# Kernel optimization log

Measured on AMD Instinct MI355X. Metric: run time of the kernel, lower is better.

The kernel has to match this reference:

```python
import jax, jax.numpy as jnp
import numpy as np
from math import pi

RADIUS = 40.0  # radius_scale
B, N = 1, 512


def map_polar_sqr(x, y, eps=1e-9):
    r = jnp.sqrt(x * x + y * y + eps)
    cond1 = (x == 0.0) & (y == 0.0)
    cond2 = (jnp.abs(y) <= jnp.abs(x)) & (~cond1)
    sx = jnp.where(x == 0.0, 1.0, x)  # safe denominators
    sy = jnp.where(y == 0.0, 1.0, y)
    c = 4.0 / pi
    x2 = jnp.sign(x) * r
    y2 = c * jnp.sign(x) * r * jnp.arctan(y / sx)
    x3 = c * jnp.sign(y) * r * jnp.arctan(x / sy)
    y3 = jnp.sign(y) * r
    x_out = jnp.where(cond1, 0.0, jnp.where(cond2, x2, x3))
    y_out = jnp.where(cond1, 0.0, jnp.where(cond2, y2, y3))
    return x_out, y_out


def axis_weights(g, size):
    # F.grid_sample bilinear, align_corners=False, padding_mode='zeros':
    # pixel coord = ((g+1)*size - 1)/2; linear weights on floor/floor+1,
    # out-of-range taps drop to zero automatically (idx only covers 0..size-1).
    c = ((g + 1.0) * size - 1.0) * 0.5
    i0 = jnp.floor(c)
    f = c - i0
    idx = jnp.arange(size, dtype=g.dtype)
    m0 = (idx == i0[..., None]).astype(g.dtype)
    m1 = (idx == i0[..., None] + 1.0).astype(g.dtype)
    return (1.0 - f)[..., None] * m0 + f[..., None] * m1  # [..., size]


def cts_conv(kernel, field, center, feat, mask, radius):
    # kernel: [o, i, kD, kH, kW]; field/center: [b, n/m, 3]; feat: [b, n, i]; mask: [b, n, 1]
    rel = (field[:, None] - center[:, :, None]) / radius            # [b,m,n,3]
    r2 = jnp.sum(rel * rel, -1)                                     # [b,m,n]
    att = jax.nn.relu((1.0 - r2) ** 3)[..., None] * mask[:, None]   # [b,m,n,1]
    xs, ys = map_polar_sqr(rel[..., 0], rel[..., 1])
    zs = rel[..., 2]
    kD, kH, kW = kernel.shape[2:]
    # grid_sample coord order: grid x -> W (last dim), y -> H, z -> D (first spatial dim)
    wz = axis_weights(zs, kD)
    wy = axis_weights(ys, kH)
    wx = axis_weights(xs, kW)
    w = jnp.einsum('bmnz,bmny,bmnx->bmnzyx', wz, wy, wx)
    w = w.reshape(*w.shape[:3], -1)                                 # [b,m,n,g=kD*kH*kW]
    fa = feat[:, None] * att                                        # [b,m,n,i]
    # exact trilinear interp + neighbor contraction without the [b,m,n,o,i] tensor:
    t = jnp.einsum('bmng,bmni->bmgi', w, fa)                        # [b,m,g,i]
    K = kernel.reshape(kernel.shape[0], kernel.shape[1], -1)        # [o,i,g]
    return jnp.einsum('bmgi,oig->bmo', t, K)


def setup_inputs() -> dict:
    key = jax.random.key(0)
    ks = jax.random.split(key, 24)

    def kern(k, o, i):
        return (jax.random.uniform(k, (o, i, 4, 4, 4), dtype=jnp.float32) - 0.5) / float(np.sqrt(i))

    def lin(kw, kb, o, i):
        return (jax.random.normal(kw, (o, i), dtype=jnp.float32) * 0.05,
                jax.random.normal(kb, (o,), dtype=jnp.float32) * 0.05)

    p = jax.random.normal(ks[0], (B, N, 3), dtype=jnp.float32) * 20.0
    v = jax.random.normal(ks[1], (B, N, 3), dtype=jnp.float32)
    other_feats = jax.random.normal(ks[2], (B, N, 62), dtype=jnp.float32)
    fluid_mask = jnp.ones((B, N, 1), dtype=jnp.float32)

    k_fluid = kern(ks[3], 32, 66)
    Wf, bf = lin(ks[4], ks[5], 32, 66)
    k1 = kern(ks[6], 64, 64); W1, b1 = lin(ks[7], ks[8], 64, 64)
    k2 = kern(ks[9], 64, 64); W2, b2 = lin(ks[10], ks[11], 64, 64)
    k3 = kern(ks[12], 64, 64); W3, b3 = lin(ks[13], ks[14], 64, 64)
    k4 = kern(ks[15], 6, 64); W4, b4 = lin(ks[16], ks[17], 6, 64)
    return dict(p=p, v=v, other_feats=other_feats, fluid_mask=fluid_mask,
                k_fluid=k_fluid, Wf=Wf, bf=bf,
                k1=k1, W1=W1, b1=b1, k2=k2, W2=W2, b2=b2,
                k3=k3, W3=W3, b3=b3, k4=k4, W4=W4, b4=b4)


def reference(p, v, other_feats, fluid_mask, k_fluid, Wf, bf,
              k1, W1, b1, k2, W2, b2, k3, W3, b3, k4, W4, b4):
    feats0 = jnp.concatenate([jnp.ones_like(p[..., :1]), v, other_feats], -1)  # [b,n,66]
    oc = cts_conv(k_fluid, p, p, feats0, fluid_mask, RADIUS)
    od = feats0 @ Wf.T + bf
    output = jnp.concatenate([oc, od], -1)  # [b,n,64]
    for k, W, bb in ((k1, W1, b1), (k2, W2, b2), (k3, W3, b3), (k4, W4, b4)):
        h = jax.nn.relu(output)
        oc = cts_conv(k, p, p, h, fluid_mask, RADIUS)
        od = h @ W.T + bb
        if od.shape[-1] == output.shape[-1]:
            output = oc + od + output
        else:
            output = oc + od
    return output  # [b,n,6]
```

## Files before the change

kernel.cpp:

```cpp
#include <hip/hip_runtime.h>

typedef _Float16 f16;
typedef _Float16 f16x8 __attribute__((ext_vector_type(8)));
typedef float f32x4 __attribute__((ext_vector_type(4)));

#define INV_R (1.0f / 40.0f)

#define OFF_HT   0u
#define OFF_B0   81920u
#define OFF_K0   82176u
#define OFF_K1   635136u
#define OFF_K2   1167616u
#define OFF_K3   1700096u
#define OFF_K4   2232576u
#define OFF_TA   2365696u
#define OFF_TB   6789376u
#define OFF_OA   11049216u
#define OFF_OB   11180288u
#define OFF_BAR  11311360u

#define PREP_TOTAL 1231936
#define NBLK 512

__device__ __forceinline__ unsigned bar_ld(unsigned* p) {
  return __hip_atomic_load(p, __ATOMIC_RELAXED, __HIP_MEMORY_SCOPE_AGENT);
}
__device__ void gridbar(unsigned* bar, int phase) {
  __syncthreads();
  if (threadIdx.x == 0) {
    int bid = blockIdx.x;
    int xcd = bid & 7;
    unsigned* xcnt = bar + xcd * 32 + phase;
    unsigned* xrel = bar + 256 + xcd * 32 + phase;
    unsigned* gcnt = bar + 512 + phase;
    unsigned* grel = bar + 544 + phase;
    __threadfence();
    __hip_atomic_fetch_add(xcnt, 1u, __ATOMIC_RELAXED, __HIP_MEMORY_SCOPE_AGENT);
    if (bid < 8) {
      while (bar_ld(xcnt) < (NBLK / 8)) __builtin_amdgcn_s_sleep(2);
      __hip_atomic_fetch_add(gcnt, 1u, __ATOMIC_RELAXED, __HIP_MEMORY_SCOPE_AGENT);
      if (bid == 0) {
        while (bar_ld(gcnt) < 8u) __builtin_amdgcn_s_sleep(2);
        __hip_atomic_store(grel, 1u, __ATOMIC_RELAXED, __HIP_MEMORY_SCOPE_AGENT);
      } else {
        while (bar_ld(grel) == 0u) __builtin_amdgcn_s_sleep(2);
      }
      __hip_atomic_store(xrel, 1u, __ATOMIC_RELAXED, __HIP_MEMORY_SCOPE_AGENT);
    } else {
      while (bar_ld(xrel) == 0u) __builtin_amdgcn_s_sleep(4);
    }
    __threadfence();
  }
  __syncthreads();
}

__device__ __forceinline__ float feats0_val(int ch, int n, const float* v, const float* other) {
  if (ch == 0) return 1.0f;
  if (ch < 4) return v[n * 3 + (ch - 1)];
  return other[n * 62 + (ch - 4)];
}

__device__ void prep_body(const float* __restrict__ v, const float* __restrict__ other,
                          const float* __restrict__ kf, const float* __restrict__ Wf,
                          const float* __restrict__ bf,
                          const float* __restrict__ k1, const float* __restrict__ W1,
                          const float* __restrict__ k2, const float* __restrict__ W2,
                          const float* __restrict__ k3, const float* __restrict__ W3,
                          const float* __restrict__ k4, const float* __restrict__ W4,
                          char* __restrict__ ws) {
  for (int idx0 = blockIdx.x * 256 + threadIdx.x; idx0 < PREP_TOTAL; idx0 += 512 * 256) {
    int idx = idx0;
    if (idx < 40960) {
      int i = idx >> 9, n = idx & 511;
      float val = (i < 66) ? feats0_val(i, n, v, other) : 0.0f;
      ((f16*)(ws + OFF_HT))[idx] = (f16)val;
      continue;
    }
    idx -= 40960;
    if (idx < 49152) {
      int m = idx / 96, j = idx % 96;
      float val = (j < 66) ? feats0_val(j, m, v, other) : 0.0f;
      ((f16*)(ws + OFF_TA))[m * 4320 + 4224 + j] = (f16)val;
      continue;
    }
    idx -= 49152;
    if (idx < 276480) {
      int o = idx / 4320, k = idx % 4320;
      float val = 0.0f;
      if (o < 32) { if (k < 4224) val = kf[o * 4224 + k]; }
      else if (k >= 4224 && k < 4290) val = Wf[(o - 32) * 66 + (k - 4224)];
      ((f16*)(ws + OFF_K0))[idx] = (f16)val;
      continue;
    }
    idx -= 276480;
    if (idx < 798720) {
      int which = idx / 266240, e = idx % 266240;
      const float* kk = which == 0 ? k1 : (which == 1 ? k2 : k3);
      const float* WW = which == 0 ? W1 : (which == 1 ? W2 : W3);
      int o = e / 4160, k = e % 4160;
      float val = (k < 4096) ? kk[o * 4096 + k] : WW[o * 64 + (k - 4096)];
      ((f16*)(ws + OFF_K1 + (unsigned)which * 532480u))[e] = (f16)val;
      continue;
    }
    idx -= 798720;
    if (idx < 66560) {
      int o = idx / 4160, k = idx % 4160;
      float val = 0.0f;
      if (o < 6) val = (k < 4096) ? k4[o * 4096 + k] : W4[o * 64 + (k - 4096)];
      ((f16*)(ws + OFF_K4))[idx] = (f16)val;
      continue;
    }
    idx -= 66560;
    if (idx < 64) ((float*)(ws + OFF_B0))[idx] = (idx < 32) ? 0.0f : bf[idx - 32];
  }
}

__device__ __forceinline__ float atan_poly(float t) {
  float t2 = t * t;
  float p = -0.0117212f;
  p = p * t2 + 0.05265332f;
  p = p * t2 - 0.11643287f;
  p = p * t2 + 0.19354346f;
  p = p * t2 - 0.33262347f;
  p = p * t2 + 0.99997726f;
  return t * p;
}

__device__ __forceinline__ void axis_w(float g, int& i0c, int& i1c, float& w0, float& w1) {
  float c = 2.0f * g + 1.5f;
  float fl = floorf(c);
  float f = c - fl;
  int i0 = (int)fl;
  w0 = (i0 >= 0 && i0 <= 3) ? (1.0f - f) : 0.0f;
  w1 = (i0 >= -1 && i0 <= 2) ? f : 0.0f;
  i0c = min(max(i0, 0), 3);
  i1c = min(max(i0 + 1, 0), 3);
}

template<int CI, int ITILES, int KDIM>
__device__ void stage1_body(const float* __restrict__ p, const float* __restrict__ mask,
                            const f16* __restrict__ hT, f16* __restrict__ tout,
                            f16* __restrict__ Wlds) {
  int tid = threadIdx.x;
  int m = blockIdx.x;
  int4* wz4 = (int4*)Wlds;
  int4 zero4 = make_int4(0, 0, 0, 0);
  #pragma unroll
  for (int i = 0; i < 16; ++i) wz4[tid + i * 256] = zero4;
  float pmx = p[m * 3 + 0], pmy = p[m * 3 + 1], pmz = p[m * 3 + 2];
  __syncthreads();
  #pragma unroll
  for (int rep = 0; rep < 2; ++rep) {
    int n = rep * 256 + tid;
    float x = (p[n * 3 + 0] - pmx) * INV_R;
    float y = (p[n * 3 + 1] - pmy) * INV_R;
    float z = (p[n * 3 + 2] - pmz) * INV_R;
    float r2 = x * x + y * y + z * z;
    float q = 1.0f - r2;
    float att = (q > 0.0f) ? q * q * q * mask[n] : 0.0f;
    bool c1 = (x == 0.0f) && (y == 0.0f);
    bool c2 = (fabsf(y) <= fabsf(x)) && !c1;
    float r = sqrtf(x * x + y * y + 1e-9f);
    float num = c2 ? y : x;
    float den = c2 ? x : y;
    float a = atan_poly(num / den);
    float s2 = copysignf(r, x), s3 = copysignf(r, y);
    const float C4PI = 1.2732395447351628f;
    float xs = c1 ? 0.0f : (c2 ? s2 : C4PI * s3 * a);
    float ys = c1 ? 0.0f : (c2 ? C4PI * s2 * a : s3);
    float zs = z;
    int iz0, iz1, iy0, iy1, ix0, ix1;
    float wz0, wz1, wy0, wy1, wx0, wx1;
    axis_w(zs, iz0, iz1, wz0, wz1);
    axis_w(ys, iy0, iy1, wy0, wy1);
    axis_w(xs, ix0, ix1, wx0, wx1);
    wz0 *= att; wz1 *= att;
    int gz[2] = {iz0 * 16, iz1 * 16};
    int gy[2] = {iy0 * 4, iy1 * 4};
    int gx[2] = {ix0, ix1};
    float wzv[2] = {wz0, wz1}, wyv[2] = {wy0, wy1}, wxv[2] = {wx0, wx1};
    #pragma unroll
    for (int za = 0; za < 2; ++za)
      #pragma unroll
      for (int ya = 0; ya < 2; ++ya)
        #pragma unroll
        for (int xa = 0; xa < 2; ++xa) {
          float w = wzv[za] * wyv[ya] * wxv[xa];
          if (w != 0.0f) {
            int g = gz[za] + gy[ya] + gx[xa];
            Wlds[g * 512 + (n ^ ((g & 7) << 3))] = (f16)w;
          }
        }
  }
  __syncthreads();
  int wave = tid >> 6, lane = tid & 63;
  int row = lane & 15, kgrp = lane >> 4;
  int grow = wave * 16 + row;
  f32x4 acc[ITILES];
  #pragma unroll
  for (int it = 0; it < ITILES; ++it) acc[it] = f32x4{0.f, 0.f, 0.f, 0.f};
  for (int k0 = 0; k0 < 512; k0 += 32) {
    int n0 = k0 + kgrp * 8;
    f16x8 afrag = *(f16x8*)&Wlds[grow * 512 + (n0 ^ ((grow & 7) << 3))];
    #pragma unroll
    for (int it = 0; it < ITILES; ++it) {
      int icol = it * 16 + row;
      f16x8 bfrag = *(const f16x8*)&hT[icol * 512 + n0];
      acc[it] = __builtin_amdgcn_mfma_f32_16x16x32_f16(afrag, bfrag, acc[it], 0, 0, 0);
    }
  }
  int g4 = wave * 16 + kgrp * 4;
  #pragma unroll
  for (int it = 0; it < ITILES; ++it) {
    int icol = it * 16 + row;
    if (icol < CI) {
      union { f16 h[4]; ushort4 u; } cv;
      #pragma unroll
      for (int r = 0; r < 4; ++r) cv.h[r] = (f16)acc[it][r];
      *(ushort4*)&tout[(size_t)m * KDIM + icol * 64 + g4] = cv.u;
    }
  }
}

template<int KDIM, bool RES, bool FINAL>
__device__ void stage2_body(const f16* __restrict__ t, const f16* __restrict__ Kf,
                            const float* __restrict__ bias, const float* __restrict__ res,
                            float* __restrict__ out32, f16* __restrict__ hT,
                            f16* __restrict__ tnext, float* __restrict__ dout,
                            float* __restrict__ red) {
  int b = blockIdx.x;
  if (b >= 128) return;
  int mtile = b >> 2, otile = b & 3;
  constexpr int KSTEPS = KDIM / 32;
  int tid = threadIdx.x;
  int kpart = tid >> 6, lane = tid & 63;
  int row = lane & 15, kgrp = lane >> 4;
  int mrow = mtile * 16 + row;
  int ocol = otile * 16 + row;
  f32x4 acc = {0.f, 0.f, 0.f, 0.f};
  for (int ks = kpart; ks < KSTEPS; ks += 4) {
    int k0 = ks * 32 + kgrp * 8;
    f16x8 afrag = *(const f16x8*)&t[(size_t)mrow * KDIM + k0];
    f16x8 bfrag = *(const f16x8*)&Kf[(size_t)ocol * KDIM + k0];
    acc = __builtin_amdgcn_mfma_f32_16x16x32_f16(afrag, bfrag, acc, 0, 0, 0);
  }
  if (kpart > 0) {
    #pragma unroll
    for (int r = 0; r < 4; ++r)
      red[(kpart - 1) * 256 + (kgrp * 4 + r) * 16 + row] = acc[r];
  }
  __syncthreads();
  if (kpart == 0) {
    #pragma unroll
    for (int kw = 0; kw < 3; ++kw)
      #pragma unroll
      for (int r = 0; r < 4; ++r)
        acc[r] += red[kw * 256 + (kgrp * 4 + r) * 16 + row];
    #pragma unroll
    for (int r = 0; r < 4; ++r) {
      int mm = mtile * 16 + kgrp * 4 + r;
      int oo = otile * 16 + row;
      if (FINAL) {
        if (oo < 6) dout[mm * 6 + oo] = acc[r] + bias[oo];
      } else {
        float val = acc[r] + bias[oo];
        if (RES) val += res[mm * 64 + oo];
        out32[mm * 64 + oo] = val;
        float h = fmaxf(val, 0.0f);
        hT[oo * 512 + mm] = (f16)h;
        tnext[(size_t)mm * 4160 + 4096 + oo] = (f16)h;
      }
    }
  }
}

__global__ __launch_bounds__(256, 2) void mega_kernel(
    const float* p, const float* v, const float* other, const float* mask,
    const float* kf, const float* Wf, const float* bf,
    const float* k1, const float* W1, const float* b1,
    const float* k2, const float* W2, const float* b2,
    const float* k3, const float* W3, const float* b3,
    const float* k4, const float* W4, const float* b4,
    float* dout, char* ws) {
  __shared__ int4 smem4[4096];
  f16* Wlds = (f16*)smem4;
  float* red = (float*)smem4;
  unsigned* bar = (unsigned*)(ws + OFF_BAR);

  f16* hT        = (f16*)(ws + OFF_HT);
  float* bias0   = (float*)(ws + OFF_B0);
  const f16* K0p = (const f16*)(ws + OFF_K0);
  const f16* K1p = (const f16*)(ws + OFF_K1);
  const f16* K2p = (const f16*)(ws + OFF_K2);
  const f16* K3p = (const f16*)(ws + OFF_K3);
  const f16* K4p = (const f16*)(ws + OFF_K4);
  f16* tA   = (f16*)(ws + OFF_TA);
  f16* tB   = (f16*)(ws + OFF_TB);
  float* outA = (float*)(ws + OFF_OA);
  float* outB = (float*)(ws + OFF_OB);

  prep_body(v, other, kf, Wf, bf, k1, W1, k2, W2, k3, W3, k4, W4, ws);
  gridbar(bar, 0);
  stage1_body<66, 5, 4320>(p, mask, hT, tA, Wlds);
  gridbar(bar, 1);
  stage2_body<4320, false, false>(tA, K0p, bias0, nullptr, outA, hT, tB, nullptr, red);
  gridbar(bar, 2);
  stage1_body<64, 4, 4160>(p, mask, hT, tB, Wlds);
  gridbar(bar, 3);
  stage2_body<4160, true, false>(tB, K1p, b1, outA, outB, hT, tA, nullptr, red);
  gridbar(bar, 4);
  stage1_body<64, 4, 4160>(p, mask, hT, tA, Wlds);
  gridbar(bar, 5);
  stage2_body<4160, true, false>(tA, K2p, b2, outB, outA, hT, tB, nullptr, red);
  gridbar(bar, 6);
  stage1_body<64, 4, 4160>(p, mask, hT, tB, Wlds);
  gridbar(bar, 7);
  stage2_body<4160, true, false>(tB, K3p, b3, outA, outB, hT, tA, nullptr, red);
  gridbar(bar, 8);
  stage1_body<64, 4, 4160>(p, mask, hT, tA, Wlds);
  gridbar(bar, 9);
  stage2_body<4160, false, true>(tA, K4p, b4, nullptr, nullptr, nullptr, nullptr, dout, red);
}

__global__ void prep_kernel_g(const float* v, const float* other,
                              const float* kf, const float* Wf, const float* bf,
                              const float* k1, const float* W1,
                              const float* k2, const float* W2,
                              const float* k3, const float* W3,
                              const float* k4, const float* W4, char* ws) {
  prep_body(v, other, kf, Wf, bf, k1, W1, k2, W2, k3, W3, k4, W4, ws);
}

template<int CI, int ITILES, int KDIM>
__global__ __launch_bounds__(256) void stage1_kernel_g(const float* p, const float* mask,
                                                       const f16* hT, f16* tout) {
  __shared__ int4 smem4[4096];
  stage1_body<CI, ITILES, KDIM>(p, mask, hT, tout, (f16*)smem4);
}

template<int KDIM, bool RES, bool FINAL>
__global__ __launch_bounds__(256) void stage2_kernel_g(const f16* t, const f16* Kf,
                                                       const float* bias, const float* res,
                                                       float* out32, f16* hT, f16* tnext,
                                                       float* dout) {
  __shared__ float red[3 * 256];
  stage2_body<KDIM, RES, FINAL>(t, Kf, bias, res, out32, hT, tnext, dout, red);
}

extern "C" void kernel_launch(void* const* d_in, const int* in_sizes, int n_in,
                              void* d_out, int out_size, void* d_ws, size_t ws_size,
                              hipStream_t stream) {
  const float* p     = (const float*)d_in[0];
  const float* v     = (const float*)d_in[1];
  const float* other = (const float*)d_in[2];
  const float* mask  = (const float*)d_in[3];
  const float* kf    = (const float*)d_in[4];
  const float* Wf    = (const float*)d_in[5];
  const float* bf    = (const float*)d_in[6];
  const float* k1    = (const float*)d_in[7];
  const float* W1    = (const float*)d_in[8];
  const float* b1    = (const float*)d_in[9];
  const float* k2    = (const float*)d_in[10];
  const float* W2    = (const float*)d_in[11];
  const float* b2    = (const float*)d_in[12];
  const float* k3    = (const float*)d_in[13];
  const float* W3    = (const float*)d_in[14];
  const float* b3    = (const float*)d_in[15];
  const float* k4    = (const float*)d_in[16];
  const float* W4    = (const float*)d_in[17];
  const float* b4    = (const float*)d_in[18];
  float* dout = (float*)d_out;
  char* ws = (char*)d_ws;
  (void)in_sizes; (void)n_in; (void)out_size; (void)ws_size;

  f16* hT        = (f16*)(ws + OFF_HT);
  float* bias0   = (float*)(ws + OFF_B0);
  const f16* K0p = (const f16*)(ws + OFF_K0);
  const f16* K1p = (const f16*)(ws + OFF_K1);
  const f16* K2p = (const f16*)(ws + OFF_K2);
  const f16* K3p = (const f16*)(ws + OFF_K3);
  const f16* K4p = (const f16*)(ws + OFF_K4);
  f16* tA   = (f16*)(ws + OFF_TA);
  f16* tB   = (f16*)(ws + OFF_TB);
  float* outA = (float*)(ws + OFF_OA);
  float* outB = (float*)(ws + OFF_OB);

  int maxb = 0;
  hipError_t e1 = hipOccupancyMaxActiveBlocksPerMultiprocessor(
      &maxb, (const void*)mega_kernel, 256, 0);
  if (e1 == hipSuccess && maxb >= 2) {
    hipMemsetAsync(ws + OFF_BAR, 0, 2304, stream);
    void* args[] = {
      (void*)&p, (void*)&v, (void*)&other, (void*)&mask,
      (void*)&kf, (void*)&Wf, (void*)&bf,
      (void*)&k1, (void*)&W1, (void*)&b1,
      (void*)&k2, (void*)&W2, (void*)&b2,
      (void*)&k3, (void*)&W3, (void*)&b3,
      (void*)&k4, (void*)&W4, (void*)&b4,
      (void*)&dout, (void*)&ws
    };
    hipError_t e2 = hipLaunchCooperativeKernel((const void*)mega_kernel, dim3(NBLK),
                                               dim3(256), args, 0, stream);
    if (e2 == hipSuccess) return;
  }

  prep_kernel_g<<<512, 256, 0, stream>>>(v, other, kf, Wf, bf, k1, W1, k2, W2,
                                         k3, W3, k4, W4, ws);
  stage1_kernel_g<66, 5, 4320><<<512, 256, 0, stream>>>(p, mask, hT, tA);
  stage2_kernel_g<4320, false, false><<<128, 256, 0, stream>>>(tA, K0p, bias0, nullptr,
                                                               outA, hT, tB, nullptr);
  stage1_kernel_g<64, 4, 4160><<<512, 256, 0, stream>>>(p, mask, hT, tB);
  stage2_kernel_g<4160, true, false><<<128, 256, 0, stream>>>(tB, K1p, b1, outA,
                                                              outB, hT, tA, nullptr);
  stage1_kernel_g<64, 4, 4160><<<512, 256, 0, stream>>>(p, mask, hT, tA);
  stage2_kernel_g<4160, true, false><<<128, 256, 0, stream>>>(tA, K2p, b2, outB,
                                                              outA, hT, tB, nullptr);
  stage1_kernel_g<64, 4, 4160><<<512, 256, 0, stream>>>(p, mask, hT, tB);
  stage2_kernel_g<4160, true, false><<<128, 256, 0, stream>>>(tB, K3p, b3, outA,
                                                              outB, hT, tA, nullptr);
  stage1_kernel_g<64, 4, 4160><<<512, 256, 0, stream>>>(p, mask, hT, tA);
  stage2_kernel_g<4160, false, true><<<128, 256, 0, stream>>>(tA, K4p, b4, nullptr,
                                                              nullptr, nullptr, nullptr, dout);
}
```

Baseline: 187.3 us.

## Fuse per-layer gather and kernel contraction into one stage with LDS-resident intermediates

```diff
diff --git a/kernel.cpp b/kernel.cpp
--- a/kernel.cpp
+++ b/kernel.cpp
@@ -1,26 +1,25 @@
 #include <hip/hip_runtime.h>
 
 typedef _Float16 f16;
+typedef _Float16 f16x2 __attribute__((ext_vector_type(2)));
 typedef _Float16 f16x8 __attribute__((ext_vector_type(8)));
 typedef float f32x4 __attribute__((ext_vector_type(4)));
 
 #define INV_R (1.0f / 40.0f)
-
-#define OFF_HT   0u
-#define OFF_B0   81920u
-#define OFF_K0   82176u
-#define OFF_K1   635136u
-#define OFF_K2   1167616u
-#define OFF_K3   1700096u
-#define OFF_K4   2232576u
-#define OFF_TA   2365696u
-#define OFF_TB   6789376u
-#define OFF_OA   11049216u
-#define OFF_OB   11180288u
-#define OFF_BAR  11311360u
-
-#define PREP_TOTAL 1231936
-#define NBLK 512
+#define NBLK 256
+
+#define OFF_HTA  0u
+#define OFF_HTB  81920u
+#define OFF_KT0  163840u
+#define OFF_KT1  720896u
+#define OFF_KT2  1253376u
+#define OFF_KT3  1785856u
+#define OFF_KT4  2318336u
+#define OFF_HG   2850816u
+#define OFF_OG   2916352u
+#define OFF_BAR  3047424u
+
+#define PREP_TOTAL 1384448
 
 __device__ __forceinline__ unsigned bar_ld(unsigned* p) {
   return __hip_atomic_load(p, __ATOMIC_RELAXED, __HIP_MEMORY_SCOPE_AGENT);
@@ -59,62 +58,6 @@
   if (ch < 4) return v[n * 3 + (ch - 1)];
   return other[n * 62 + (ch - 4)];
 }
-
-__device__ void prep_body(const float* __restrict__ v, const float* __restrict__ other,
-                          const float* __restrict__ kf, const float* __restrict__ Wf,
-                          const float* __restrict__ bf,
-                          const float* __restrict__ k1, const float* __restrict__ W1,
-                          const float* __restrict__ k2, const float* __restrict__ W2,
-                          const float* __restrict__ k3, const float* __restrict__ W3,
-                          const float* __restrict__ k4, const float* __restrict__ W4,
-                          char* __restrict__ ws) {
-  for (int idx0 = blockIdx.x * 256 + threadIdx.x; idx0 < PREP_TOTAL; idx0 += 512 * 256) {
-    int idx = idx0;
-    if (idx < 40960) {
-      int i = idx >> 9, n = idx & 511;
-      float val = (i < 66) ? feats0_val(i, n, v, other) : 0.0f;
-      ((f16*)(ws + OFF_HT))[idx] = (f16)val;
-      continue;
-    }
-    idx -= 40960;
-    if (idx < 49152) {
-      int m = idx / 96, j = idx % 96;
-      float val = (j < 66) ? feats0_val(j, m, v, other) : 0.0f;
-      ((f16*)(ws + OFF_TA))[m * 4320 + 4224 + j] = (f16)val;
-      continue;
-    }
-    idx -= 49152;
-    if (idx < 276480) {
-      int o = idx / 4320, k = idx % 4320;
-      float val = 0.0f;
-      if (o < 32) { if (k < 4224) val = kf[o * 4224 + k]; }
-      else if (k >= 4224 && k < 4290) val = Wf[(o - 32) * 66 + (k - 4224)];
-      ((f16*)(ws + OFF_K0))[idx] = (f16)val;
-      continue;
-    }
-    idx -= 276480;
-    if (idx < 798720) {
-      int which = idx / 266240, e = idx % 266240;
-      const float* kk = which == 0 ? k1 : (which == 1 ? k2 : k3);
-      const float* WW = which == 0 ? W1 : (which == 1 ? W2 : W3);
-      int o = e / 4160, k = e % 4160;
-      float val = (k < 4096) ? kk[o * 4096 + k] : WW[o * 64 + (k - 4096)];
-      ((f16*)(ws + OFF_K1 + (unsigned)which * 532480u))[e] = (f16)val;
-      continue;
-    }
-    idx -= 798720;
-    if (idx < 66560) {
-      int o = idx / 4160, k = idx % 4160;
-      float val = 0.0f;
-      if (o < 6) val = (k < 4096) ? k4[o * 4096 + k] : W4[o * 64 + (k - 4096)];
-      ((f16*)(ws + OFF_K4))[idx] = (f16)val;
-      continue;
-    }
-    idx -= 66560;
-    if (idx < 64) ((float*)(ws + OFF_B0))[idx] = (idx < 32) ? 0.0f : bf[idx - 32];
-  }
-}
-
 __device__ __forceinline__ float atan_poly(float t) {
   float t2 = t * t;
   float p = -0.0117212f;
@@ -125,7 +68,6 @@
   p = p * t2 + 0.99997726f;
   return t * p;
 }
-
 __device__ __forceinline__ void axis_w(float g, int& i0c, int& i1c, float& w0, float& w1) {
   float c = 2.0f * g + 1.5f;
   float fl = floorf(c);
@@ -136,145 +78,213 @@
   i0c = min(max(i0, 0), 3);
   i1c = min(max(i0 + 1, 0), 3);
 }
-
-template<int CI, int ITILES, int KDIM>
-__device__ void stage1_body(const float* __restrict__ p, const float* __restrict__ mask,
-                            const f16* __restrict__ hT, f16* __restrict__ tout,
-                            f16* __restrict__ Wlds) {
-  int tid = threadIdx.x;
-  int m = blockIdx.x;
-  int4* wz4 = (int4*)Wlds;
-  int4 zero4 = make_int4(0, 0, 0, 0);
+__device__ __forceinline__ float dot2f(f16x2 a, f16x2 b, float c) {
+#if defined(__has_builtin) && __has_builtin(__builtin_amdgcn_fdot2)
+  return __builtin_amdgcn_fdot2(a, b, c, false);
+#else
+  return c + (float)a[0] * (float)b[0] + (float)a[1] * (float)b[1];
+#endif
+}
+
+__device__ void prep_body(const float* __restrict__ v, const float* __restrict__ other,
+                          const float* __restrict__ kf, const float* __restrict__ Wf,
+                          const float* __restrict__ k1, const float* __restrict__ W1,
+                          const float* __restrict__ k2, const float* __restrict__ W2,
+                          const float* __restrict__ k3, const float* __restrict__ W3,
+                          const float* __restrict__ k4, const float* __restrict__ W4,
+                          char* __restrict__ ws) {
+  f16* hTA = (f16*)(ws + OFF_HTA);
+  for (int idx = blockIdx.x * 256 + threadIdx.x; idx < PREP_TOTAL; idx += NBLK * 256) {
+    int e = idx;
+    if (e < 40960) {
+      int i = e >> 9, n = e & 511;
+      hTA[e] = (f16)((i < 66) ? feats0_val(i, n, v, other) : 0.0f);
+      continue;
+    }
+    e -= 40960;
+    if (e < 278528) {
+      int o = (e >> 3) & 63;
+      int k = ((e >> 9) << 3) + (e & 7);
+      float val = 0.0f;
+      if (k < 4224) { if (o < 32) val = kf[o * 4224 + k]; }
+      else if (k < 4290) { if (o >= 32) val = Wf[(o - 32) * 66 + (k - 4224)]; }
+      ((f16*)(ws + OFF_KT0))[e] = (f16)val;
+      continue;
+    }
+    e -= 278528;
+    if (e < 798720) {
+      int which = e / 266240, ee = e % 266240;
+      const float* kk = which == 0 ? k1 : (which == 1 ? k2 : k3);
+      const float* WW = which == 0 ? W1 : (which == 1 ? W2 : W3);
+      int o = (ee >> 3) & 63;
+      int k = ((ee >> 9) << 3) + (ee & 7);
+      float val = (k < 4096) ? kk[o * 4096 + k] : WW[o * 64 + (k - 4096)];
+      ((f16*)(ws + OFF_KT1))[(size_t)which * 266240 + ee] = (f16)val;
+      continue;
+    }
+    e -= 798720;
+    {
+      int o = (e >> 3) & 63;
+      int k = ((e >> 9) << 3) + (e & 7);
+      float val = 0.0f;
+      if (o < 6) val = (k < 4096) ? k4[o * 4096 + k] : W4[o * 64 + (k - 4096)];
+      ((f16*)(ws + OFF_KT4))[e] = (f16)val;
+    }
+  }
+}
+
+template<int LAYER>
+__device__ void layer_body(const float* __restrict__ p, const float* __restrict__ mask,
+                           const float* __restrict__ v, const float* __restrict__ other,
+                           const float* __restrict__ bias, const f16* __restrict__ KT,
+                           const f16* __restrict__ hT_in, f16* __restrict__ hT_out,
+                           f16* __restrict__ hG, float* __restrict__ outG,
+                           float* __restrict__ dout,
+                           f16* __restrict__ Wl, f16* __restrict__ tt, float* __restrict__ red) {
+  constexpr int CI     = (LAYER == 0) ? 66 : 64;
+  constexpr int ITILES = (LAYER == 0) ? 5 : 4;
+  constexpr int KD     = (LAYER == 0) ? 4352 : 4160;
+  constexpr bool RES   = (LAYER >= 1 && LAYER <= 3);
+  constexpr bool FINAL = (LAYER == 4);
+  const int tid = threadIdx.x;
+  const int b = blockIdx.x;
+  const int wave = tid >> 6, lane = tid & 63;
+  const int row = lane & 15, kgrp = lane >> 4;
+  const int grow = wave * 16 + row;
+
   #pragma unroll
-  for (int i = 0; i < 16; ++i) wz4[tid + i * 256] = zero4;
-  float pmx = p[m * 3 + 0], pmy = p[m * 3 + 1], pmz = p[m * 3 + 2];
-  __syncthreads();
-  #pragma unroll
-  for (int rep = 0; rep < 2; ++rep) {
-    int n = rep * 256 + tid;
-    float x = (p[n * 3 + 0] - pmx) * INV_R;
-    float y = (p[n * 3 + 1] - pmy) * INV_R;
-    float z = (p[n * 3 + 2] - pmz) * INV_R;
-    float r2 = x * x + y * y + z * z;
-    float q = 1.0f - r2;
-    float att = (q > 0.0f) ? q * q * q * mask[n] : 0.0f;
-    bool c1 = (x == 0.0f) && (y == 0.0f);
-    bool c2 = (fabsf(y) <= fabsf(x)) && !c1;
-    float r = sqrtf(x * x + y * y + 1e-9f);
-    float num = c2 ? y : x;
-    float den = c2 ? x : y;
-    float a = atan_poly(num / den);
-    float s2 = copysignf(r, x), s3 = copysignf(r, y);
-    const float C4PI = 1.2732395447351628f;
-    float xs = c1 ? 0.0f : (c2 ? s2 : C4PI * s3 * a);
-    float ys = c1 ? 0.0f : (c2 ? C4PI * s2 * a : s3);
-    float zs = z;
-    int iz0, iz1, iy0, iy1, ix0, ix1;
-    float wz0, wz1, wy0, wy1, wx0, wx1;
-    axis_w(zs, iz0, iz1, wz0, wz1);
-    axis_w(ys, iy0, iy1, wy0, wy1);
-    axis_w(xs, ix0, ix1, wx0, wx1);
-    wz0 *= att; wz1 *= att;
-    int gz[2] = {iz0 * 16, iz1 * 16};
-    int gy[2] = {iy0 * 4, iy1 * 4};
-    int gx[2] = {ix0, ix1};
-    float wzv[2] = {wz0, wz1}, wyv[2] = {wy0, wy1}, wxv[2] = {wx0, wx1};
+  for (int mi = 0; mi < 2; ++mi) {
+    const int m = b + mi * NBLK;
+    const float pmx = p[m * 3 + 0], pmy = p[m * 3 + 1], pmz = p[m * 3 + 2];
+    f32x4 acc[ITILES];
     #pragma unroll
-    for (int za = 0; za < 2; ++za)
+    for (int it = 0; it < ITILES; ++it) acc[it] = f32x4{0.f, 0.f, 0.f, 0.f};
+
+    #pragma unroll
+    for (int half = 0; half < 2; ++half) {
+      __syncthreads();
+      int4* w4 = (int4*)Wl;
+      int4 z4 = make_int4(0, 0, 0, 0);
       #pragma unroll
-      for (int ya = 0; ya < 2; ++ya)
+      for (int i = 0; i < 8; ++i) w4[tid + i * 256] = z4;
+      __syncthreads();
+      {
+        const int n = half * 256 + tid;
+        float x = (p[n * 3 + 0] - pmx) * INV_R;
+        float y = (p[n * 3 + 1] - pmy) * INV_R;
+        float z = (p[n * 3 + 2] - pmz) * INV_R;
+        float r2 = x * x + y * y + z * z;
+        float q = 1.0f - r2;
+        float att = (q > 0.0f) ? q * q * q * mask[n] : 0.0f;
+        bool c1 = (x == 0.0f) && (y == 0.0f);
+        bool c2 = (fabsf(y) <= fabsf(x)) && !c1;
+        float r = sqrtf(x * x + y * y + 1e-9f);
+        float num = c2 ? y : x;
+        float den = c2 ? x : y;
+        float a = atan_poly(num / den);
+        float s2 = copysignf(r, x), s3 = copysignf(r, y);
+        const float C4PI = 1.2732395447351628f;
+        float xs = c1 ? 0.0f : (c2 ? s2 : C4PI * s3 * a);
+        float ys = c1 ? 0.0f : (c2 ? C4PI * s2 * a : s3);
+        float zs = z;
+        int iz0, iz1, iy0, iy1, ix0, ix1;
+        float wz0, wz1, wy0, wy1, wx0, wx1;
+        axis_w(zs, iz0, iz1, wz0, wz1);
+        axis_w(ys, iy0, iy1, wy0, wy1);
+        axis_w(xs, ix0, ix1, wx0, wx1);
+        wz0 *= att; wz1 *= att;
+        int gz[2] = {iz0 * 16, iz1 * 16};
+        int gy[2] = {iy0 * 4, iy1 * 4};
+        int gx[2] = {ix0, ix1};
+        float wzv[2] = {wz0, wz1}, wyv[2] = {wy0, wy1}, wxv[2] = {wx0, wx1};
         #pragma unroll
-        for (int xa = 0; xa < 2; ++xa) {
-          float w = wzv[za] * wyv[ya] * wxv[xa];
-          if (w != 0.0f) {
-            int g = gz[za] + gy[ya] + gx[xa];
-            Wlds[g * 512 + (n ^ ((g & 7) << 3))] = (f16)w;
-          }
+        for (int za = 0; za < 2; ++za)
+          #pragma unroll
+          for (int ya = 0; ya < 2; ++ya)
+            #pragma unroll
+            for (int xa = 0; xa < 2; ++xa) {
+              float w = wzv[za] * wyv[ya] * wxv[xa];
+              if (w != 0.0f) {
+                int g = gz[za] + gy[ya] + gx[xa];
+                Wl[g * 256 + (tid ^ ((g & 7) << 3))] = (f16)w;
+              }
+            }
+      }
+      __syncthreads();
+      #pragma unroll
+      for (int k0 = 0; k0 < 8; ++k0) {
+        const int n0l = k0 * 32 + kgrp * 8;
+        f16x8 afrag = *(f16x8*)&Wl[grow * 256 + (n0l ^ ((grow & 7) << 3))];
+        #pragma unroll
+        for (int it = 0; it < ITILES; ++it) {
+          f16x8 bfrag = *(const f16x8*)&hT_in[(it * 16 + row) * 512 + half * 256 + n0l];
+          acc[it] = __builtin_amdgcn_mfma_f32_16x16x32_f16(afrag, bfrag, acc[it], 0, 0, 0);
         }
-  }
-  __syncthreads();
-  int wave = tid >> 6, lane = tid & 63;
-  int row = lane & 15, kgrp = lane >> 4;
-  int grow = wave * 16 + row;
-  f32x4 acc[ITILES];
-  #pragma unroll
-  for (int it = 0; it < ITILES; ++it) acc[it] = f32x4{0.f, 0.f, 0.f, 0.f};
-  for (int k0 = 0; k0 < 512; k0 += 32) {
-    int n0 = k0 + kgrp * 8;
-    f16x8 afrag = *(f16x8*)&Wlds[grow * 512 + (n0 ^ ((grow & 7) << 3))];
+      }
+    }
+    const int g4 = wave * 16 + kgrp * 4;
     #pragma unroll
     for (int it = 0; it < ITILES; ++it) {
-      int icol = it * 16 + row;
-      f16x8 bfrag = *(const f16x8*)&hT[icol * 512 + n0];
-      acc[it] = __builtin_amdgcn_mfma_f32_16x16x32_f16(afrag, bfrag, acc[it], 0, 0, 0);
-    }
-  }
-  int g4 = wave * 16 + kgrp * 4;
-  #pragma unroll
-  for (int it = 0; it < ITILES; ++it) {
-    int icol = it * 16 + row;
-    if (icol < CI) {
-      union { f16 h[4]; ushort4 u; } cv;
+      const int icol = it * 16 + row;
+      if (icol < CI) {
+        union { f16 h[4]; short4 s; } cv;
+        #pragma unroll
+        for (int r = 0; r < 4; ++r) cv.h[r] = (f16)acc[it][r];
+        *(short4*)&tt[mi * 4352 + icol * 64 + g4] = cv.s;
+      }
+    }
+    if (LAYER == 0) {
+      if (tid < 128)
+        tt[mi * 4352 + 4224 + tid] = (f16)((tid < 66) ? feats0_val(tid, m, v, other) : 0.0f);
+    } else {
+      if (tid < 64) tt[mi * 4352 + 4096 + tid] = hG[m * 64 + tid];
+    }
+  }
+  __syncthreads();
+
+  constexpr int GPS = KD / 32;
+  {
+    const int o = tid & 63, wv = tid >> 6;
+    float a0 = 0.f, a1 = 0.f;
+    const f16* kp  = KT + ((size_t)(wv * GPS) * 64 + o) * 8;
+    const f16* t0p = tt + (size_t)(wv * GPS) * 8;
+    const f16* t1p = tt + 4352 + (size_t)(wv * GPS) * 8;
+    for (int g = 0; g < GPS; ++g) {
+      union { f16x8 v8; f16x2 p2[4]; } uk, u0, u1;
+      uk.v8 = *(const f16x8*)kp;
+      u0.v8 = *(const f16x8*)t0p;
+      u1.v8 = *(const f16x8*)t1p;
+      kp += 512; t0p += 8; t1p += 8;
       #pragma unroll
-      for (int r = 0; r < 4; ++r) cv.h[r] = (f16)acc[it][r];
-      *(ushort4*)&tout[(size_t)m * KDIM + icol * 64 + g4] = cv.u;
-    }
-  }
-}
-
-template<int KDIM, bool RES, bool FINAL>
-__device__ void stage2_body(const f16* __restrict__ t, const f16* __restrict__ Kf,
-                            const float* __restrict__ bias, const float* __restrict__ res,
-                            float* __restrict__ out32, f16* __restrict__ hT,
-                            f16* __restrict__ tnext, float* __restrict__ dout,
-                            float* __restrict__ red) {
-  int b = blockIdx.x;
-  if (b >= 128) return;
-  int mtile = b >> 2, otile = b & 3;
-  constexpr int KSTEPS = KDIM / 32;
-  int tid = threadIdx.x;
-  int kpart = tid >> 6, lane = tid & 63;
-  int row = lane & 15, kgrp = lane >> 4;
-  int mrow = mtile * 16 + row;
-  int ocol = otile * 16 + row;
-  f32x4 acc = {0.f, 0.f, 0.f, 0.f};
-  for (int ks = kpart; ks < KSTEPS; ks += 4) {
-    int k0 = ks * 32 + kgrp * 8;
-    f16x8 afrag = *(const f16x8*)&t[(size_t)mrow * KDIM + k0];
-    f16x8 bfrag = *(const f16x8*)&Kf[(size_t)ocol * KDIM + k0];
-    acc = __builtin_amdgcn_mfma_f32_16x16x32_f16(afrag, bfrag, acc, 0, 0, 0);
-  }
-  if (kpart > 0) {
-    #pragma unroll
-    for (int r = 0; r < 4; ++r)
-      red[(kpart - 1) * 256 + (kgrp * 4 + r) * 16 + row] = acc[r];
+      for (int j = 0; j < 4; ++j) {
+        a0 = dot2f(uk.p2[j], u0.p2[j], a0);
+        a1 = dot2f(uk.p2[j], u1.p2[j], a1);
+      }
+    }
+    red[wv * 128 + o]      = a0;
+    red[wv * 128 + 64 + o] = a1;
   }
   __syncthreads();
-  if (kpart == 0) {
-    #pragma unroll
-    for (int kw = 0; kw < 3; ++kw)
-      #pragma unroll
-      for (int r = 0; r < 4; ++r)
-        acc[r] += red[kw * 256 + (kgrp * 4 + r) * 16 + row];
-    #pragma unroll
-    for (int r = 0; r < 4; ++r) {
-      int mm = mtile * 16 + kgrp * 4 + r;
-      int oo = otile * 16 + row;
-      if (FINAL) {
-        if (oo < 6) dout[mm * 6 + oo] = acc[r] + bias[oo];
-      } else {
-        float val = acc[r] + bias[oo];
-        if (RES) val += res[mm * 64 + oo];
-        out32[mm * 64 + oo] = val;
-        float h = fmaxf(val, 0.0f);
-        hT[oo * 512 + mm] = (f16)h;
-        tnext[(size_t)mm * 4160 + 4096 + oo] = (f16)h;
-      }
-    }
-  }
-}
-
-__global__ __launch_bounds__(256, 2) void mega_kernel(
+  if (tid < 128) {
+    const int mi = tid >> 6, oo = tid & 63;
+    const int m = b + mi * NBLK;
+    float s = red[mi * 64 + oo] + red[128 + mi * 64 + oo]
+            + red[256 + mi * 64 + oo] + red[384 + mi * 64 + oo];
+    if (FINAL) {
+      if (oo < 6) dout[m * 6 + oo] = s + bias[oo];
+    } else {
+      float bb = (LAYER == 0) ? ((oo < 32) ? 0.0f : bias[oo - 32]) : bias[oo];
+      float val = s + bb;
+      if (RES) val += outG[m * 64 + oo];
+      outG[m * 64 + oo] = val;
+      float h = fmaxf(val, 0.0f);
+      hG[m * 64 + oo] = (f16)h;
+      hT_out[oo * 512 + m] = (f16)h;
+    }
+  }
+}
+
+__global__ __launch_bounds__(256) void mega_kernel(
     const float* p, const float* v, const float* other, const float* mask,
     const float* kf, const float* Wf, const float* bf,
     const float* k1, const float* W1, const float* b1,
@@ -282,69 +292,47 @@
     const float* k3, const float* W3, const float* b3,
     const float* k4, const float* W4, const float* b4,
     float* dout, char* ws) {
-  __shared__ int4 smem4[4096];
-  f16* Wlds = (f16*)smem4;
-  float* red = (float*)smem4;
+  __shared__ int4 blob[3264];
+  f16* Wl = (f16*)blob;
+  f16* tt = Wl + 16384;
+  float* red = (float*)(tt + 8704);
   unsigned* bar = (unsigned*)(ws + OFF_BAR);
 
-  f16* hT        = (f16*)(ws + OFF_HT);
-  float* bias0   = (float*)(ws + OFF_B0);
-  const f16* K0p = (const f16*)(ws + OFF_K0);
-  const f16* K1p = (const f16*)(ws + OFF_K1);
-  const f16* K2p = (const f16*)(ws + OFF_K2);
-  const f16* K3p = (const f16*)(ws + OFF_K3);
-  const f16* K4p = (const f16*)(ws + OFF_K4);
-  f16* tA   = (f16*)(ws + OFF_TA);
-  f16* tB   = (f16*)(ws + OFF_TB);
-  float* outA = (float*)(ws + OFF_OA);
-  float* outB = (float*)(ws + OFF_OB);
-
-  prep_body(v, other, kf, Wf, bf, k1, W1, k2, W2, k3, W3, k4, W4, ws);
+  f16* hTA = (f16*)(ws + OFF_HTA);
+  f16* hTB = (f16*)(ws + OFF_HTB);
+  f16* hG  = (f16*)(ws + OFF_HG);
+  float* outG = (float*)(ws + OFF_OG);
+
+  prep_body(v, other, kf, Wf, k1, W1, k2, W2, k3, W3, k4, W4, ws);
   gridbar(bar, 0);
-  stage1_body<66, 5, 4320>(p, mask, hT, tA, Wlds);
+  layer_body<0>(p, mask, v, other, bf, (const f16*)(ws + OFF_KT0), hTA, hTB, hG, outG, nullptr, Wl, tt, red);
   gridbar(bar, 1);
-  stage2_body<4320, false, false>(tA, K0p, bias0, nullptr, outA, hT, tB, nullptr, red);
+  layer_body<1>(p, mask, v, other, b1, (const f16*)(ws + OFF_KT1), hTB, hTA, hG, outG, nullptr, Wl, tt, red);
   gridbar(bar, 2);
-  stage1_body<64, 4, 4160>(p, mask, hT, tB, Wlds);
+  layer_body<2>(p, mask, v, other, b2, (const f16*)(ws + OFF_KT2), hTA, hTB, hG, outG, nullptr, Wl, tt, red);
   gridbar(bar, 3);
-  stage2_body<4160, true, false>(tB, K1p, b1, outA, outB, hT, tA, nullptr, red);
+  layer_body<3>(p, mask, v, other, b3, (const f16*)(ws + OFF_KT3), hTB, hTA, hG, outG, nullptr, Wl, tt, red);
   gridbar(bar, 4);
-  stage1_body<64, 4, 4160>(p, mask, hT, tA, Wlds);
-  gridbar(bar, 5);
-  stage2_body<4160, true, false>(tA, K2p, b2, outB, outA, hT, tB, nullptr, red);
-  gridbar(bar, 6);
-  stage1_body<64, 4, 4160>(p, mask, hT, tB, Wlds);
-  gridbar(bar, 7);
-  stage2_body<4160, true, false>(tB, K3p, b3, outA, outB, hT, tA, nullptr, red);
-  gridbar(bar, 8);
-  stage1_body<64, 4, 4160>(p, mask, hT, tA, Wlds);
-  gridbar(bar, 9);
-  stage2_body<4160, false, true>(tA, K4p, b4, nullptr, nullptr, nullptr, nullptr, dout, red);
-}
-
-__global__ void prep_kernel_g(const float* v, const float* other,
-                              const float* kf, const float* Wf, const float* bf,
-                              const float* k1, const float* W1,
-                              const float* k2, const float* W2,
-                              const float* k3, const float* W3,
-                              const float* k4, const float* W4, char* ws) {
-  prep_body(v, other, kf, Wf, bf, k1, W1, k2, W2, k3, W3, k4, W4, ws);
-}
-
-template<int CI, int ITILES, int KDIM>
-__global__ __launch_bounds__(256) void stage1_kernel_g(const float* p, const float* mask,
-                                                       const f16* hT, f16* tout) {
-  __shared__ int4 smem4[4096];
-  stage1_body<CI, ITILES, KDIM>(p, mask, hT, tout, (f16*)smem4);
-}
-
-template<int KDIM, bool RES, bool FINAL>
-__global__ __launch_bounds__(256) void stage2_kernel_g(const f16* t, const f16* Kf,
-                                                       const float* bias, const float* res,
-                                                       float* out32, f16* hT, f16* tnext,
-                                                       float* dout) {
-  __shared__ float red[3 * 256];
-  stage2_body<KDIM, RES, FINAL>(t, Kf, bias, res, out32, hT, tnext, dout, red);
+  layer_body<4>(p, mask, v, other, b4, (const f16*)(ws + OFF_KT4), hTA, nullptr, hG, outG, dout, Wl, tt, red);
+}
+
+__global__ __launch_bounds__(256) void prep_g(
+    const float* v, const float* other, const float* kf, const float* Wf,
+    const float* k1, const float* W1, const float* k2, const float* W2,
+    const float* k3, const float* W3, const float* k4, const float* W4, char* ws) {
+  prep_body(v, other, kf, Wf, k1, W1, k2, W2, k3, W3, k4, W4, ws);
+}
+
+template<int LAYER>
+__global__ __launch_bounds__(256) void layer_g(
+    const float* p, const float* mask, const float* v, const float* other,
+    const float* bias, const f16* KT, const f16* hT_in, f16* hT_out,
+    f16* hG, float* outG, float* dout) {
+  __shared__ int4 blob[3264];
+  f16* Wl = (f16*)blob;
+  f16* tt = Wl + 16384;
+  float* red = (float*)(tt + 8704);
+  layer_body<LAYER>(p, mask, v, other, bias, KT, hT_in, hT_out, hG, outG, dout, Wl, tt, red);
 }
 
 extern "C" void kernel_launch(void* const* d_in, const int* in_sizes, int n_in,
@@ -373,22 +361,20 @@
   char* ws = (char*)d_ws;
   (void)in_sizes; (void)n_in; (void)out_size; (void)ws_size;
 
-  f16* hT        = (f16*)(ws + OFF_HT);
-  float* bias0   = (float*)(ws + OFF_B0);
-  const f16* K0p = (const f16*)(ws + OFF_K0);
-  const f16* K1p = (const f16*)(ws + OFF_K1);
-  const f16* K2p = (const f16*)(ws + OFF_K2);
-  const f16* K3p = (const f16*)(ws + OFF_K3);
-  const f16* K4p = (const f16*)(ws + OFF_K4);
-  f16* tA   = (f16*)(ws + OFF_TA);
-  f16* tB   = (f16*)(ws + OFF_TB);
-  float* outA = (float*)(ws + OFF_OA);
-  float* outB = (float*)(ws + OFF_OB);
+  const f16* KT0 = (const f16*)(ws + OFF_KT0);
+  const f16* KT1 = (const f16*)(ws + OFF_KT1);
+  const f16* KT2 = (const f16*)(ws + OFF_KT2);
+  const f16* KT3 = (const f16*)(ws + OFF_KT3);
+  const f16* KT4c = (const f16*)(ws + OFF_KT4);
+  f16* hTA = (f16*)(ws + OFF_HTA);
+  f16* hTB = (f16*)(ws + OFF_HTB);
+  f16* hG  = (f16*)(ws + OFF_HG);
+  float* outG = (float*)(ws + OFF_OG);
 
   int maxb = 0;
   hipError_t e1 = hipOccupancyMaxActiveBlocksPerMultiprocessor(
       &maxb, (const void*)mega_kernel, 256, 0);
-  if (e1 == hipSuccess && maxb >= 2) {
+  if (e1 == hipSuccess && maxb >= 1) {
     hipMemsetAsync(ws + OFF_BAR, 0, 2304, stream);
     void* args[] = {
       (void*)&p, (void*)&v, (void*)&other, (void*)&mask,
@@ -404,21 +390,10 @@
     if (e2 == hipSuccess) return;
   }
 
-  prep_kernel_g<<<512, 256, 0, stream>>>(v, other, kf, Wf, bf, k1, W1, k2, W2,
-                                         k3, W3, k4, W4, ws);
-  stage1_kernel_g<66, 5, 4320><<<512, 256, 0, stream>>>(p, mask, hT, tA);
-  stage2_kernel_g<4320, false, false><<<128, 256, 0, stream>>>(tA, K0p, bias0, nullptr,
-                                                               outA, hT, tB, nullptr);
-  stage1_kernel_g<64, 4, 4160><<<512, 256, 0, stream>>>(p, mask, hT, tB);
-  stage2_kernel_g<4160, true, false><<<128, 256, 0, stream>>>(tB, K1p, b1, outA,
-                                                              outB, hT, tA, nullptr);
-  stage1_kernel_g<64, 4, 4160><<<512, 256, 0, stream>>>(p, mask, hT, tA);
-  stage2_kernel_g<4160, true, false><<<128, 256, 0, stream>>>(tA, K2p, b2, outB,
-                                                              outA, hT, tB, nullptr);
-  stage1_kernel_g<64, 4, 4160><<<512, 256, 0, stream>>>(p, mask, hT, tB);
-  stage2_kernel_g<4160, true, false><<<128, 256, 0, stream>>>(tB, K3p, b3, outA,
-                                                              outB, hT, tA, nullptr);
-  stage1_kernel_g<64, 4, 4160><<<512, 256, 0, stream>>>(p, mask, hT, tA);
-  stage2_kernel_g<4160, false, true><<<128, 256, 0, stream>>>(tA, K4p, b4, nullptr,
-                                                              nullptr, nullptr, nullptr, dout);
-}
+  prep_g<<<NBLK, 256, 0, stream>>>(v, other, kf, Wf, k1, W1, k2, W2, k3, W3, k4, W4, ws);
+  layer_g<0><<<NBLK, 256, 0, stream>>>(p, mask, v, other, bf, KT0, hTA, hTB, hG, outG, nullptr);
+  layer_g<1><<<NBLK, 256, 0, stream>>>(p, mask, v, other, b1, KT1, hTB, hTA, hG, outG, nullptr);
+  layer_g<2><<<NBLK, 256, 0, stream>>>(p, mask, v, other, b2, KT2, hTA, hTB, hG, outG, nullptr);
+  layer_g<3><<<NBLK, 256, 0, stream>>>(p, mask, v, other, b3, KT3, hTB, hTA, hG, outG, nullptr);
+  layer_g<4><<<NBLK, 256, 0, stream>>>(p, mask, v, other, b4, KT4c, hTA, nullptr, hG, outG, dout);
+}
```

New measurement: 202.1 us. +7.9%, slower.
